# Kernel optimization log

Measured on AMD Instinct MI355X. Metric: run time of the kernel, lower is better.

## Reference

```python
import jax, jax.numpy as jnp
import numpy as np

SIGMA = 1.0
EPS = 1e-5
NEG = 0.1
CPG = 16  # channels_per_group


def bn(x, g, b):
    # batch norm over the point dimension (training-mode batch stats)
    m = x.mean(0, keepdims=True)
    v = x.var(0, keepdims=True)
    return (x - m) / jnp.sqrt(v + EPS) * g + b


def lrelu(x):
    return jnp.where(x >= 0, x, NEG * x)


def kpinv_conv(q_pts, s_pts, x, idx, kp, w_g1, b_g1, w_g2, b_g2):
    # KPInv: neighbor gather + kernel-point influence weighting + dynamically
    # generated (involution-style) per-point, per-kernel, per-group weights.
    M, H = idx.shape
    K = kp.shape[0]
    C = x.shape[1]
    G = C // CPG
    # shadow padding: far-away point, zero feature
    s_pts_p = jnp.concatenate([s_pts, jnp.full((1, s_pts.shape[1]), 1e6, s_pts.dtype)], 0)
    x_p = jnp.concatenate([x, jnp.zeros((1, C), x.dtype)], 0)
    npts = s_pts_p[idx] - q_pts[:, None, :]              # (M,H,D) relative neighbor positions
    nfeat = x_p[idx]                                      # (M,H,C) gathered neighbor features
    # squared distances to kernel points without materializing (M,H,K,D)
    d2 = ((npts ** 2).sum(-1)[:, :, None]
          + (kp ** 2).sum(-1)[None, None, :]
          - 2.0 * jnp.einsum('mhd,kd->mhk', npts, kp))    # (M,H,K)
    # linear influence, sum aggregation
    infl = jnp.clip(1.0 - jnp.sqrt(jnp.maximum(d2, 0.0)) / SIGMA, 0.0, None)
    fk = jnp.einsum('mhk,mhc->mkc', infl, nfeat)          # (M,K,C) per-kernel aggregated feats
    # generate conv weights from local max-pooled center feature
    center = jnp.max(nfeat, axis=1)                       # (M,C)
    w = lrelu(center @ w_g1 + b_g1) @ w_g2 + b_g2         # (M,K*G)
    w = w.reshape(M, K, G)
    fk = fk.reshape(M, K, G, CPG)
    return jnp.einsum('mkg,mkgc->mgc', w, fk).reshape(M, C)


def setup_inputs() -> dict:
    key = jax.random.key(0)
    ks = jax.random.split(key, 10)
    M, H, Cin, Cmid, K, D = 50000, 32, 128, 32, 15, 3
    R = 2.5
    pts = jax.random.uniform(ks[0], (M, D), dtype=jnp.float32) * 10.0
    return dict(
        q_pts=pts,
        s_pts=pts,
        s_feats=jax.random.normal(ks[1], (M, Cin), dtype=jnp.float32),
        neighbor_indices=jax.random.randint(ks[2], (M, H), 0, M),
        kernel_points=jax.random.normal(ks[3], (K, D), dtype=jnp.float32) * (0.3 * R),
        w_u1=jax.random.normal(ks[4], (Cin, Cmid), dtype=jnp.float32) / np.float32(np.sqrt(Cin)),
        g_u1=jnp.ones((Cmid,), jnp.float32), b_u1=jnp.zeros((Cmid,), jnp.float32),
        w_g1=jax.random.normal(ks[5], (Cmid, Cmid // 4), dtype=jnp.float32) / np.float32(np.sqrt(Cmid)),
        b_g1=jnp.zeros((Cmid // 4,), jnp.float32),
        w_g2=jax.random.normal(ks[6], (Cmid // 4, K * (Cmid // CPG)), dtype=jnp.float32) / np.float32(np.sqrt(Cmid // 4)),
        b_g2=jnp.zeros((K * (Cmid // CPG),), jnp.float32),
        g_c=jnp.ones((Cmid,), jnp.float32), b_c=jnp.zeros((Cmid,), jnp.float32),
        w_u2=jax.random.normal(ks[7], (Cmid, Cin), dtype=jnp.float32) / np.float32(np.sqrt(Cmid)),
        g_u2=jnp.ones((Cin,), jnp.float32), b_u2=jnp.zeros((Cin,), jnp.float32),
    )


def reference(q_pts, s_pts, s_feats, neighbor_indices, kernel_points,
              w_u1, g_u1, b_u1, w_g1, b_g1, w_g2, b_g2,
              g_c, b_c, w_u2, g_u2, b_u2):
    # unary1: linear -> BN -> LeakyReLU (in_channels != mid_channels)
    x = lrelu(bn(s_feats @ w_u1, g_u1, b_u1))
    # KPInv conv block: conv -> BN -> LeakyReLU
    x = kpinv_conv(q_pts, s_pts, x, neighbor_indices, kernel_points, w_g1, b_g1, w_g2, b_g2)
    x = lrelu(bn(x, g_c, b_c))
    # unary2: linear -> BN (no activation)
    x = bn(x @ w_u2, g_u2, b_u2)
    # not strided, in==out: shortcut is identity on s_feats
    return lrelu(x + s_feats)
```

## Files before the change

kernel.cpp:

```cpp
#include <hip/hip_runtime.h>

#define CMID 32
#define CIN 128
#define HNB 32
#define KP 15
#define NEG 0.1f
#define EPS 1e-5f

__global__ __launch_bounds__(256) void k1_gemm1(
    const float* __restrict__ A,
    const float* __restrict__ B,
    float* __restrict__ y1,
    float* __restrict__ st,
    int M)
{
    __shared__ __align__(16) float AsT[32 * 128];
    __shared__ __align__(16) float Bs[128 * 32];
    __shared__ __align__(16) float red[256];
    int t = threadIdx.x;
    for (int i = t; i < 128 * 32; i += 256) Bs[i] = B[i];

    int m0 = blockIdx.x * 128;
    int tx = t & 7, ty = t >> 3;
    int srow = t & 127, shh = t >> 7;
    float acc[4][4] = {{0.f}};

    for (int ch = 0; ch < 4; ++ch) {
        __syncthreads();
        int gr = m0 + srow;
        const float4* ap = (const float4*)(A + (size_t)gr * CIN + ch * 32 + shh * 16);
        float4 f0, f1, f2, f3;
        if (gr < M) { f0 = ap[0]; f1 = ap[1]; f2 = ap[2]; f3 = ap[3]; }
        else { f0 = f1 = f2 = f3 = make_float4(0.f, 0.f, 0.f, 0.f); }
        {
            int cb = shh * 16;
            AsT[(cb + 0) * 128 + srow] = f0.x;  AsT[(cb + 1) * 128 + srow] = f0.y;
            AsT[(cb + 2) * 128 + srow] = f0.z;  AsT[(cb + 3) * 128 + srow] = f0.w;
            AsT[(cb + 4) * 128 + srow] = f1.x;  AsT[(cb + 5) * 128 + srow] = f1.y;
            AsT[(cb + 6) * 128 + srow] = f1.z;  AsT[(cb + 7) * 128 + srow] = f1.w;
            AsT[(cb + 8) * 128 + srow] = f2.x;  AsT[(cb + 9) * 128 + srow] = f2.y;
            AsT[(cb + 10) * 128 + srow] = f2.z; AsT[(cb + 11) * 128 + srow] = f2.w;
            AsT[(cb + 12) * 128 + srow] = f3.x; AsT[(cb + 13) * 128 + srow] = f3.y;
            AsT[(cb + 14) * 128 + srow] = f3.z; AsT[(cb + 15) * 128 + srow] = f3.w;
        }
        __syncthreads();
        const float* bsp = Bs + (ch * 32) * 32 + tx * 4;
#pragma unroll
        for (int jl = 0; jl < 32; ++jl) {
            float4 av = *(const float4*)(AsT + jl * 128 + ty * 4);
            float4 bv = *(const float4*)(bsp + jl * 32);
            acc[0][0] += av.x * bv.x; acc[0][1] += av.x * bv.y; acc[0][2] += av.x * bv.z; acc[0][3] += av.x * bv.w;
            acc[1][0] += av.y * bv.x; acc[1][1] += av.y * bv.y; acc[1][2] += av.y * bv.z; acc[1][3] += av.y * bv.w;
            acc[2][0] += av.z * bv.x; acc[2][1] += av.z * bv.y; acc[2][2] += av.z * bv.z; acc[2][3] += av.z * bv.w;
            acc[3][0] += av.w * bv.x; acc[3][1] += av.w * bv.y; acc[3][2] += av.w * bv.z; acc[3][3] += av.w * bv.w;
        }
    }
#pragma unroll
    for (int i = 0; i < 4; ++i) {
        int r = m0 + ty * 4 + i;
        if (r < M)
            *(float4*)(y1 + (size_t)r * CMID + tx * 4) =
                make_float4(acc[i][0], acc[i][1], acc[i][2], acc[i][3]);
    }
    float s4[4], q4[4];
#pragma unroll
    for (int e = 0; e < 4; ++e) {
        s4[e] = acc[0][e] + acc[1][e] + acc[2][e] + acc[3][e];
        q4[e] = acc[0][e] * acc[0][e] + acc[1][e] * acc[1][e]
              + acc[2][e] * acc[2][e] + acc[3][e] * acc[3][e];
    }
#pragma unroll
    for (int off = 8; off <= 32; off <<= 1) {
#pragma unroll
        for (int e = 0; e < 4; ++e) {
            s4[e] += __shfl_xor(s4[e], off);
            q4[e] += __shfl_xor(q4[e], off);
        }
    }
    int lw = t >> 6, ll = t & 63;
    if (ll < 8) {
#pragma unroll
        for (int e = 0; e < 4; ++e) {
            red[(lw * 8 + ll) * 8 + e] = s4[e];
            red[(lw * 8 + ll) * 8 + 4 + e] = q4[e];
        }
    }
    __syncthreads();
    if (t < 64) {
        int tx2 = t >> 3, k = t & 7;
        float v = red[(0 * 8 + tx2) * 8 + k] + red[(1 * 8 + tx2) * 8 + k]
                + red[(2 * 8 + tx2) * 8 + k] + red[(3 * 8 + tx2) * 8 + k];
        int col = tx2 * 4 + (k & 3);
        atomicAdd(&st[(k < 4 ? 0 : 32) + col], v);
    }
}

__global__ __launch_bounds__(256, 4) void k3_kpinv(
    const float* __restrict__ y1, const float* __restrict__ st,
    const float* __restrict__ q_pts, const float* __restrict__ s_pts,
    const int* __restrict__ idx, const float* __restrict__ kp,
    const float* __restrict__ g_u1, const float* __restrict__ b_u1,
    const float* __restrict__ w_g1, const float* __restrict__ b_g1,
    const float* __restrict__ w_g2, const float* __restrict__ b_g2,
    float* __restrict__ x2, int M)
{
    __shared__ __align__(16) float a1s[32], b1s[32];
    __shared__ __align__(16) float wg1[32 * 8];
    __shared__ __align__(16) float bg1[8];
    __shared__ __align__(16) float wg2[8 * 30];
    __shared__ __align__(16) float bg2[32];
    __shared__ __align__(16) float kps[KP * 3 + 1];
    __shared__ __align__(16) float vbuf[4][2][32 * 32];
    __shared__ __align__(16) float aux[4][2][144];

    int t = threadIdx.x;
    if (t < 32) {
        float mean = st[t] * (1.0f / M);
        float var  = st[32 + t] * (1.0f / M) - mean * mean;
        float inv  = rsqrtf(var + EPS);
        float a = g_u1[t] * inv;
        a1s[t] = a;
        b1s[t] = b_u1[t] - mean * a;
    }
    wg1[t & 255] = w_g1[t & 255];
    if (t < 8)   bg1[t] = b_g1[t];
    if (t < 240) wg2[t] = w_g2[t];
    if (t < 30)  bg2[t] = b_g2[t];
    else if (t < 32) bg2[t] = 0.f;
    if (t < KP * 3) kps[t] = kp[t];
    __syncthreads();

    int wave = t >> 6, lane = t & 63;
    int p = lane >> 5;
    int q = lane & 31;
    int m = blockIdx.x * 8 + wave * 2 + p;
    bool valid = (m < M);
    int mm = valid ? m : 0;
    float* vb = &vbuf[wave][p][0];
    float* ax = &aux[wave][p][0];

    int h = q;
    int n = idx[(size_t)mm * HNB + h];
    float qx = q_pts[mm * 3 + 0], qy = q_pts[mm * 3 + 1], qz = q_pts[mm * 3 + 2];
    float dx = s_pts[n * 3 + 0] - qx;
    float dy = s_pts[n * 3 + 1] - qy;
    float dz = s_pts[n * 3 + 2] - qz;

    float infl[KP];
#pragma unroll
    for (int k = 0; k < KP; ++k) {
        float ex = dx - kps[k * 3 + 0];
        float ey = dy - kps[k * 3 + 1];
        float ez = dz - kps[k * 3 + 2];
        float d = sqrtf(ex * ex + ey * ey + ez * ez);
        infl[k] = fmaxf(1.0f - d, 0.f);
    }

    {
        const float4* row = (const float4*)(y1 + (size_t)n * CMID);
        int hq4 = h >> 2, h3 = h & 3;
#pragma unroll
        for (int jj = 0; jj < 8; ++jj) {
            float4 f = row[jj];
            float vv[4] = {f.x, f.y, f.z, f.w};
#pragma unroll
            for (int e = 0; e < 4; ++e) {
                int c = jj * 4 + e;
                float x = vv[e] * a1s[c] + b1s[c];
                x = fmaxf(x, NEG * x);
                vb[(c << 5) + ((hq4 ^ (c & 7)) << 2) + h3] = x;
            }
        }
    }
    __builtin_amdgcn_wave_barrier();

    {
        int c = q;
        int c7 = c & 7;
        const float* vrow = vb + (c << 5);
        float cm = -1e30f;
#pragma unroll
        for (int j = 0; j < 8; ++j) {
            const float4 f = *(const float4*)(vrow + ((j ^ c7) << 2));
            cm = fmaxf(fmaxf(fmaxf(cm, f.x), fmaxf(f.y, f.z)), f.w);
        }
        ax[c] = cm;
        __builtin_amdgcn_wave_barrier();

        int jm = c & 7;
        float acc = bg1[jm];
#pragma unroll
        for (int cc = 0; cc < 8; ++cc) {
            const float4 ce = *(const float4*)(ax + (cc << 2));
            acc += ce.x * wg1[(cc * 4 + 0) * 8 + jm];
            acc += ce.y * wg1[(cc * 4 + 1) * 8 + jm];
            acc += ce.z * wg1[(cc * 4 + 2) * 8 + jm];
            acc += ce.w * wg1[(cc * 4 + 3) * 8 + jm];
        }
        float h1v = fmaxf(acc, NEG * acc);
        if (c < 8) ax[32 + c] = h1v;
        __builtin_amdgcn_wave_barrier();

        float wv = 0.f;
        if (c < 30) {
            const float4 ha = *(const float4*)(ax + 32);
            const float4 hb = *(const float4*)(ax + 36);
            wv = bg2[c]
               + ha.x * wg2[0 * 30 + c] + ha.y * wg2[1 * 30 + c]
               + ha.z * wg2[2 * 30 + c] + ha.w * wg2[3 * 30 + c]
               + hb.x * wg2[4 * 30 + c] + hb.y * wg2[5 * 30 + c]
               + hb.z * wg2[6 * 30 + c] + hb.w * wg2[7 * 30 + c];
        }
        ax[40 + c] = wv;
    }
    __builtin_amdgcn_wave_barrier();

    {
        float wf[32];
#pragma unroll
        for (int j = 0; j < 8; ++j) {
            const float4 wc = *(const float4*)(ax + 40 + (j << 2));
            wf[j * 4 + 0] = wc.x; wf[j * 4 + 1] = wc.y;
            wf[j * 4 + 2] = wc.z; wf[j * 4 + 3] = wc.w;
        }
        float s0 = 0.f, s1 = 0.f;
#pragma unroll
        for (int k = 0; k < KP; ++k) {
            s0 += infl[k] * wf[2 * k + 0];
            s1 += infl[k] * wf[2 * k + 1];
        }
        ax[72 + q]  = s0;
        ax[104 + q] = s1;
    }
    __builtin_amdgcn_wave_barrier();

    {
        int c = q;
        int c7 = c & 7;
        const float* sbuf = ax + 72 + ((c >> 4) << 5);
        const float* vrow = vb + (c << 5);
        float o = 0.f;
#pragma unroll
        for (int j = 0; j < 8; ++j) {
            const float4 vv = *(const float4*)(vrow + ((j ^ c7) << 2));
            const float4 ss = *(const float4*)(sbuf + (j << 2));
            o += vv.x * ss.x + vv.y * ss.y + vv.z * ss.z + vv.w * ss.w;
        }
        if (valid) x2[(size_t)m * CMID + c] = o;
    }
}

__global__ __launch_bounds__(256) void k4_stats32(
    const float* __restrict__ x2, float* __restrict__ st, int M)
{
    int t = threadIdx.x;
    int c = t & 31;
    float sum = 0.f, sq = 0.f;
    for (int r = blockIdx.x * 8 + (t >> 5); r < M; r += gridDim.x * 8) {
        float v = x2[(size_t)r * CMID + c];
        sum += v; sq += v * v;
    }
    __shared__ float red[256];
    red[t] = sum; __syncthreads();
    if (t < 32) { float s = 0.f; for (int i = 0; i < 8; ++i) s += red[t + 32 * i]; atomicAdd(&st[64 + t], s); }
    __syncthreads();
    red[t] = sq; __syncthreads();
    if (t < 32) { float s = 0.f; for (int i = 0; i < 8; ++i) s += red[t + 32 * i]; atomicAdd(&st[96 + t], s); }
}

__global__ __launch_bounds__(256) void k6_zstats(
    const float* __restrict__ x2, const float* __restrict__ w_u2,
    const float* __restrict__ g_c, const float* __restrict__ b_c,
    float* __restrict__ st, int M)
{
    __shared__ __align__(16) float ST[32 * 128];
    __shared__ __align__(16) float Ws[32 * 32];
    __shared__ __align__(16) float acs[32], bcs[32];
    __shared__ __align__(16) float red[256];
    int t = threadIdx.x;
    int cb = blockIdx.y;
    int m0 = blockIdx.x * 128;
    if (t < 32) {
        float mean = st[64 + t] * (1.0f / M);
        float var  = st[96 + t] * (1.0f / M) - mean * mean;
        float inv  = rsqrtf(var + EPS);
        float a = g_c[t] * inv;
        acs[t] = a; bcs[t] = b_c[t] - mean * a;
    }
    for (int i = t; i < 32 * 32; i += 256)
        Ws[i] = w_u2[(i >> 5) * CIN + cb * 32 + (i & 31)];
    __syncthreads();

    int srow = t & 127, shh = t >> 7;
    int gr = m0 + srow;
    const float4* xp = (const float4*)(x2 + (size_t)gr * CMID + shh * 16);
    float4 f0, f1, f2, f3;
    if (gr < M) { f0 = xp[0]; f1 = xp[1]; f2 = xp[2]; f3 = xp[3]; }
    else { f0 = f1 = f2 = f3 = make_float4(0.f, 0.f, 0.f, 0.f); }
    {
        float vv[16] = {f0.x, f0.y, f0.z, f0.w, f1.x, f1.y, f1.z, f1.w,
                        f2.x, f2.y, f2.z, f2.w, f3.x, f3.y, f3.z, f3.w};
        int cbse = shh * 16;
#pragma unroll
        for (int e = 0; e < 16; ++e) {
            int c = cbse + e;
            float x = vv[e] * acs[c] + bcs[c];
            x = fmaxf(x, NEG * x);
            ST[c * 128 + srow] = (gr < M) ? x : 0.f;
        }
    }
    __syncthreads();

    int tx = t & 7, ty = t >> 3;
    float acc[4][4] = {{0.f}};
#pragma unroll
    for (int j = 0; j < 32; ++j) {
        float4 av = *(const float4*)(ST + j * 128 + ty * 4);
        float4 bv = *(const float4*)(Ws + j * 32 + tx * 4);
        acc[0][0] += av.x * bv.x; acc[0][1] += av.x * bv.y; acc[0][2] += av.x * bv.z; acc[0][3] += av.x * bv.w;
        acc[1][0] += av.y * bv.x; acc[1][1] += av.y * bv.y; acc[1][2] += av.y * bv.z; acc[1][3] += av.y * bv.w;
        acc[2][0] += av.z * bv.x; acc[2][1] += av.z * bv.y; acc[2][2] += av.z * bv.z; acc[2][3] += av.z * bv.w;
        acc[3][0] += av.w * bv.x; acc[3][1] += av.w * bv.y; acc[3][2] += av.w * bv.z; acc[3][3] += av.w * bv.w;
    }
    float s4[4], q4[4];
#pragma unroll
    for (int e = 0; e < 4; ++e) {
        s4[e] = acc[0][e] + acc[1][e] + acc[2][e] + acc[3][e];
        q4[e] = acc[0][e] * acc[0][e] + acc[1][e] * acc[1][e]
              + acc[2][e] * acc[2][e] + acc[3][e] * acc[3][e];
    }
#pragma unroll
    for (int off = 8; off <= 32; off <<= 1) {
#pragma unroll
        for (int e = 0; e < 4; ++e) {
            s4[e] += __shfl_xor(s4[e], off);
            q4[e] += __shfl_xor(q4[e], off);
        }
    }
    int lw = t >> 6, ll = t & 63;
    if (ll < 8) {
#pragma unroll
        for (int e = 0; e < 4; ++e) {
            red[(lw * 8 + ll) * 8 + e] = s4[e];
            red[(lw * 8 + ll) * 8 + 4 + e] = q4[e];
        }
    }
    __syncthreads();
    if (t < 64) {
        int tx2 = t >> 3, k = t & 7;
        float v = red[(0 * 8 + tx2) * 8 + k] + red[(1 * 8 + tx2) * 8 + k]
                + red[(2 * 8 + tx2) * 8 + k] + red[(3 * 8 + tx2) * 8 + k];
        int col = cb * 32 + tx2 * 4 + (k & 3);
        atomicAdd(&st[(k < 4 ? 128 : 256) + col], v);
    }
}

__global__ __launch_bounds__(256) void k8_final(
    const float* __restrict__ x2, const float* __restrict__ w_u2,
    const float* __restrict__ g_c, const float* __restrict__ b_c,
    const float* __restrict__ g_u2, const float* __restrict__ b_u2,
    const float* __restrict__ s_feats, const float* __restrict__ st,
    float* __restrict__ out, int M)
{
    __shared__ __align__(16) float ST[32 * 128];
    __shared__ __align__(16) float Ws[32 * 32];
    __shared__ __align__(16) float acs[32], bcs[32];
    __shared__ __align__(16) float a2s[32], b2s[32];
    int t = threadIdx.x;
    int cb = blockIdx.y;
    int m0 = blockIdx.x * 128;
    if (t < 32) {
        float mean = st[64 + t] * (1.0f / M);
        float var  = st[96 + t] * (1.0f / M) - mean * mean;
        float inv  = rsqrtf(var + EPS);
        float a = g_c[t] * inv;
        acs[t] = a; bcs[t] = b_c[t] - mean * a;
        int c = cb * 32 + t;
        float mean2 = st[128 + c] * (1.0f / M);
        float var2  = st[256 + c] * (1.0f / M) - mean2 * mean2;
        float inv2  = rsqrtf(var2 + EPS);
        float a2 = g_u2[c] * inv2;
        a2s[t] = a2; b2s[t] = b_u2[c] - mean2 * a2;
    }
    for (int i = t; i < 32 * 32; i += 256)
        Ws[i] = w_u2[(i >> 5) * CIN + cb * 32 + (i & 31)];
    __syncthreads();

    int srow = t & 127, shh = t >> 7;
    int gr = m0 + srow;
    const float4* xp = (const float4*)(x2 + (size_t)gr * CMID + shh * 16);
    float4 f0, f1, f2, f3;
    if (gr < M) { f0 = xp[0]; f1 = xp[1]; f2 = xp[2]; f3 = xp[3]; }
    else { f0 = f1 = f2 = f3 = make_float4(0.f, 0.f, 0.f, 0.f); }
    {
        float vv[16] = {f0.x, f0.y, f0.z, f0.w, f1.x, f1.y, f1.z, f1.w,
                        f2.x, f2.y, f2.z, f2.w, f3.x, f3.y, f3.z, f3.w};
        int cbse = shh * 16;
#pragma unroll
        for (int e = 0; e < 16; ++e) {
            int c = cbse + e;
            float x = vv[e] * acs[c] + bcs[c];
            x = fmaxf(x, NEG * x);
            ST[c * 128 + srow] = (gr < M) ? x : 0.f;
        }
    }
    __syncthreads();

    int tx = t & 7, ty = t >> 3;
    float acc[4][4] = {{0.f}};
#pragma unroll
    for (int j = 0; j < 32; ++j) {
        float4 av = *(const float4*)(ST + j * 128 + ty * 4);
        float4 bv = *(const float4*)(Ws + j * 32 + tx * 4);
        acc[0][0] += av.x * bv.x; acc[0][1] += av.x * bv.y; acc[0][2] += av.x * bv.z; acc[0][3] += av.x * bv.w;
        acc[1][0] += av.y * bv.x; acc[1][1] += av.y * bv.y; acc[1][2] += av.y * bv.z; acc[1][3] += av.y * bv.w;
        acc[2][0] += av.z * bv.x; acc[2][1] += av.z * bv.y; acc[2][2] += av.z * bv.z; acc[2][3] += av.z * bv.w;
        acc[3][0] += av.w * bv.x; acc[3][1] += av.w * bv.y; acc[3][2] += av.w * bv.z; acc[3][3] += av.w * bv.w;
    }
    int lc = tx * 4;
    float a0 = a2s[lc + 0], a1 = a2s[lc + 1], a2v = a2s[lc + 2], a3 = a2s[lc + 3];
    float bb0 = b2s[lc + 0], bb1 = b2s[lc + 1], bb2 = b2s[lc + 2], bb3 = b2s[lc + 3];
#pragma unroll
    for (int i = 0; i < 4; ++i) {
        int r = m0 + ty * 4 + i;
        if (r < M) {
            size_t gi = (size_t)r * CIN + cb * 32 + lc;
            float4 sf = *(const float4*)(s_feats + gi);
            float v0 = acc[i][0] * a0 + bb0 + sf.x;
            float v1 = acc[i][1] * a1 + bb1 + sf.y;
            float v2 = acc[i][2] * a2v + bb2 + sf.z;
            float v3 = acc[i][3] * a3 + bb3 + sf.w;
            v0 = fmaxf(v0, NEG * v0); v1 = fmaxf(v1, NEG * v1);
            v2 = fmaxf(v2, NEG * v2); v3 = fmaxf(v3, NEG * v3);
            *(float4*)(out + gi) = make_float4(v0, v1, v2, v3);
        }
    }
}

extern "C" void kernel_launch(void* const* d_in, const int* in_sizes, int n_in,
                              void* d_out, int out_size, void* d_ws, size_t ws_size,
                              hipStream_t stream) {
    const float* q_pts   = (const float*)d_in[0];
    const float* s_pts   = (const float*)d_in[1];
    const float* s_feats = (const float*)d_in[2];
    const int*   idx     = (const int*)d_in[3];
    const float* kp      = (const float*)d_in[4];
    const float* w_u1    = (const float*)d_in[5];
    const float* g_u1    = (const float*)d_in[6];
    const float* b_u1    = (const float*)d_in[7];
    const float* w_g1    = (const float*)d_in[8];
    const float* b_g1    = (const float*)d_in[9];
    const float* w_g2    = (const float*)d_in[10];
    const float* b_g2    = (const float*)d_in[11];
    const float* g_c     = (const float*)d_in[12];
    const float* b_c     = (const float*)d_in[13];
    const float* w_u2    = (const float*)d_in[14];
    const float* g_u2    = (const float*)d_in[15];
    const float* b_u2    = (const float*)d_in[16];

    int M = in_sizes[3] / HNB;

    float* ws = (float*)d_ws;
    float* y1 = ws;
    float* x2 = ws + (size_t)M * CMID;
    float* st = ws + (size_t)M * 2 * CMID;

    hipMemsetAsync(st, 0, 384 * sizeof(float), stream);

    int nbr = (M + 127) / 128;
    k1_gemm1<<<nbr, 256, 0, stream>>>(s_feats, w_u1, y1, st, M);
    k3_kpinv<<<(M + 7) / 8, 256, 0, stream>>>(y1, st, q_pts, s_pts, idx, kp,
                                              g_u1, b_u1, w_g1, b_g1, w_g2, b_g2,
                                              x2, M);
    k4_stats32<<<128, 256, 0, stream>>>(x2, st, M);
    k6_zstats<<<dim3(nbr, 4), 256, 0, stream>>>(x2, w_u2, g_c, b_c, st, M);
    k8_final<<<dim3(nbr, 4), 256, 0, stream>>>(x2, w_u2, g_c, b_c, g_u2, b_u2,
                                               s_feats, st, (float*)d_out, M);
}
```

Before: 253.0 us.

## Fuse all stages into one persistent kernel with software grid barriers

Replaces the five separate kernel launches with a single persistent kernel of fixed grid size that loops over row tiles in each phase. The phases are separated by atomic-counter grid barriers, and the shared-memory buffers for each phase are overlaid in a union. This is meant to remove launch gaps and kernel-boundary drains. In exchange it relies on all blocks being co-resident, since otherwise the barriers deadlock, and it loses parallelism in phases that previously used far more blocks.

```diff
diff --git a/kernel.cpp b/kernel.cpp
--- a/kernel.cpp
+++ b/kernel.cpp
@@ -6,433 +6,441 @@
 #define KP 15
 #define NEG 0.1f
 #define EPS 1e-5f
-
-__global__ __launch_bounds__(256) void k1_gemm1(
-    const float* __restrict__ A,
-    const float* __restrict__ B,
-    float* __restrict__ y1,
-    float* __restrict__ st,
-    int M)
+#define GRID 512
+#define GQ (GRID / 4)
+
+__device__ __forceinline__ void grid_barrier(unsigned int* bar, unsigned int target, int t)
 {
-    __shared__ __align__(16) float AsT[32 * 128];
-    __shared__ __align__(16) float Bs[128 * 32];
-    __shared__ __align__(16) float red[256];
-    int t = threadIdx.x;
-    for (int i = t; i < 128 * 32; i += 256) Bs[i] = B[i];
-
-    int m0 = blockIdx.x * 128;
-    int tx = t & 7, ty = t >> 3;
-    int srow = t & 127, shh = t >> 7;
-    float acc[4][4] = {{0.f}};
-
-    for (int ch = 0; ch < 4; ++ch) {
-        __syncthreads();
-        int gr = m0 + srow;
-        const float4* ap = (const float4*)(A + (size_t)gr * CIN + ch * 32 + shh * 16);
-        float4 f0, f1, f2, f3;
-        if (gr < M) { f0 = ap[0]; f1 = ap[1]; f2 = ap[2]; f3 = ap[3]; }
-        else { f0 = f1 = f2 = f3 = make_float4(0.f, 0.f, 0.f, 0.f); }
-        {
-            int cb = shh * 16;
-            AsT[(cb + 0) * 128 + srow] = f0.x;  AsT[(cb + 1) * 128 + srow] = f0.y;
-            AsT[(cb + 2) * 128 + srow] = f0.z;  AsT[(cb + 3) * 128 + srow] = f0.w;
-            AsT[(cb + 4) * 128 + srow] = f1.x;  AsT[(cb + 5) * 128 + srow] = f1.y;
-            AsT[(cb + 6) * 128 + srow] = f1.z;  AsT[(cb + 7) * 128 + srow] = f1.w;
-            AsT[(cb + 8) * 128 + srow] = f2.x;  AsT[(cb + 9) * 128 + srow] = f2.y;
-            AsT[(cb + 10) * 128 + srow] = f2.z; AsT[(cb + 11) * 128 + srow] = f2.w;
-            AsT[(cb + 12) * 128 + srow] = f3.x; AsT[(cb + 13) * 128 + srow] = f3.y;
-            AsT[(cb + 14) * 128 + srow] = f3.z; AsT[(cb + 15) * 128 + srow] = f3.w;
-        }
-        __syncthreads();
-        const float* bsp = Bs + (ch * 32) * 32 + tx * 4;
-#pragma unroll
-        for (int jl = 0; jl < 32; ++jl) {
-            float4 av = *(const float4*)(AsT + jl * 128 + ty * 4);
-            float4 bv = *(const float4*)(bsp + jl * 32);
-            acc[0][0] += av.x * bv.x; acc[0][1] += av.x * bv.y; acc[0][2] += av.x * bv.z; acc[0][3] += av.x * bv.w;
-            acc[1][0] += av.y * bv.x; acc[1][1] += av.y * bv.y; acc[1][2] += av.y * bv.z; acc[1][3] += av.y * bv.w;
-            acc[2][0] += av.z * bv.x; acc[2][1] += av.z * bv.y; acc[2][2] += av.z * bv.z; acc[2][3] += av.z * bv.w;
-            acc[3][0] += av.w * bv.x; acc[3][1] += av.w * bv.y; acc[3][2] += av.w * bv.z; acc[3][3] += av.w * bv.w;
-        }
-    }
-#pragma unroll
-    for (int i = 0; i < 4; ++i) {
-        int r = m0 + ty * 4 + i;
-        if (r < M)
-            *(float4*)(y1 + (size_t)r * CMID + tx * 4) =
-                make_float4(acc[i][0], acc[i][1], acc[i][2], acc[i][3]);
-    }
-    float s4[4], q4[4];
-#pragma unroll
-    for (int e = 0; e < 4; ++e) {
-        s4[e] = acc[0][e] + acc[1][e] + acc[2][e] + acc[3][e];
-        q4[e] = acc[0][e] * acc[0][e] + acc[1][e] * acc[1][e]
-              + acc[2][e] * acc[2][e] + acc[3][e] * acc[3][e];
-    }
-#pragma unroll
-    for (int off = 8; off <= 32; off <<= 1) {
-#pragma unroll
-        for (int e = 0; e < 4; ++e) {
-            s4[e] += __shfl_xor(s4[e], off);
-            q4[e] += __shfl_xor(q4[e], off);
-        }
-    }
-    int lw = t >> 6, ll = t & 63;
-    if (ll < 8) {
-#pragma unroll
-        for (int e = 0; e < 4; ++e) {
-            red[(lw * 8 + ll) * 8 + e] = s4[e];
-            red[(lw * 8 + ll) * 8 + 4 + e] = q4[e];
-        }
+    __threadfence();
+    __syncthreads();
+    if (t == 0) {
+        __hip_atomic_fetch_add(bar, 1u, __ATOMIC_RELEASE, __HIP_MEMORY_SCOPE_AGENT);
+        while (__hip_atomic_load(bar, __ATOMIC_ACQUIRE, __HIP_MEMORY_SCOPE_AGENT) < target)
+            __builtin_amdgcn_s_sleep(8);
     }
     __syncthreads();
-    if (t < 64) {
-        int tx2 = t >> 3, k = t & 7;
-        float v = red[(0 * 8 + tx2) * 8 + k] + red[(1 * 8 + tx2) * 8 + k]
-                + red[(2 * 8 + tx2) * 8 + k] + red[(3 * 8 + tx2) * 8 + k];
-        int col = tx2 * 4 + (k & 3);
-        atomicAdd(&st[(k < 4 ? 0 : 32) + col], v);
-    }
 }
 
-__global__ __launch_bounds__(256, 4) void k3_kpinv(
-    const float* __restrict__ y1, const float* __restrict__ st,
+struct SA {
+    float AsT[32 * 128];
+    float Bs[128 * 32];
+    float red[256];
+};
+struct SB {
+    float a1s[32], b1s[32];
+    float wg1[32 * 8];
+    float bg1[8];
+    float wg2[8 * 30];
+    float bg2[32];
+    float kps[48];
+    float vbuf[4][2][1024];
+    float aux[4][2][144];
+};
+struct SD {
+    float ST[32 * 128];
+    float Ws[32 * 32];
+    float acs[32], bcs[32];
+    float a2s[32], b2s[32];
+    float red[256];
+};
+union SU { SA a; SB b; SD d; };
+
+__global__ __launch_bounds__(256, 3) void fused(
     const float* __restrict__ q_pts, const float* __restrict__ s_pts,
-    const int* __restrict__ idx, const float* __restrict__ kp,
-    const float* __restrict__ g_u1, const float* __restrict__ b_u1,
+    const float* __restrict__ s_feats, const int* __restrict__ idx,
+    const float* __restrict__ kp,
+    const float* __restrict__ w_u1, const float* __restrict__ g_u1,
+    const float* __restrict__ b_u1,
     const float* __restrict__ w_g1, const float* __restrict__ b_g1,
     const float* __restrict__ w_g2, const float* __restrict__ b_g2,
-    float* __restrict__ x2, int M)
-{
-    __shared__ __align__(16) float a1s[32], b1s[32];
-    __shared__ __align__(16) float wg1[32 * 8];
-    __shared__ __align__(16) float bg1[8];
-    __shared__ __align__(16) float wg2[8 * 30];
-    __shared__ __align__(16) float bg2[32];
-    __shared__ __align__(16) float kps[KP * 3 + 1];
-    __shared__ __align__(16) float vbuf[4][2][32 * 32];
-    __shared__ __align__(16) float aux[4][2][144];
-
-    int t = threadIdx.x;
-    if (t < 32) {
-        float mean = st[t] * (1.0f / M);
-        float var  = st[32 + t] * (1.0f / M) - mean * mean;
-        float inv  = rsqrtf(var + EPS);
-        float a = g_u1[t] * inv;
-        a1s[t] = a;
-        b1s[t] = b_u1[t] - mean * a;
-    }
-    wg1[t & 255] = w_g1[t & 255];
-    if (t < 8)   bg1[t] = b_g1[t];
-    if (t < 240) wg2[t] = w_g2[t];
-    if (t < 30)  bg2[t] = b_g2[t];
-    else if (t < 32) bg2[t] = 0.f;
-    if (t < KP * 3) kps[t] = kp[t];
-    __syncthreads();
-
-    int wave = t >> 6, lane = t & 63;
-    int p = lane >> 5;
-    int q = lane & 31;
-    int m = blockIdx.x * 8 + wave * 2 + p;
-    bool valid = (m < M);
-    int mm = valid ? m : 0;
-    float* vb = &vbuf[wave][p][0];
-    float* ax = &aux[wave][p][0];
-
-    int h = q;
-    int n = idx[(size_t)mm * HNB + h];
-    float qx = q_pts[mm * 3 + 0], qy = q_pts[mm * 3 + 1], qz = q_pts[mm * 3 + 2];
-    float dx = s_pts[n * 3 + 0] - qx;
-    float dy = s_pts[n * 3 + 1] - qy;
-    float dz = s_pts[n * 3 + 2] - qz;
-
-    float infl[KP];
-#pragma unroll
-    for (int k = 0; k < KP; ++k) {
-        float ex = dx - kps[k * 3 + 0];
-        float ey = dy - kps[k * 3 + 1];
-        float ez = dz - kps[k * 3 + 2];
-        float d = sqrtf(ex * ex + ey * ey + ez * ez);
-        infl[k] = fmaxf(1.0f - d, 0.f);
-    }
-
-    {
-        const float4* row = (const float4*)(y1 + (size_t)n * CMID);
-        int hq4 = h >> 2, h3 = h & 3;
-#pragma unroll
-        for (int jj = 0; jj < 8; ++jj) {
-            float4 f = row[jj];
-            float vv[4] = {f.x, f.y, f.z, f.w};
-#pragma unroll
-            for (int e = 0; e < 4; ++e) {
-                int c = jj * 4 + e;
-                float x = vv[e] * a1s[c] + b1s[c];
-                x = fmaxf(x, NEG * x);
-                vb[(c << 5) + ((hq4 ^ (c & 7)) << 2) + h3] = x;
-            }
-        }
-    }
-    __builtin_amdgcn_wave_barrier();
-
-    {
-        int c = q;
-        int c7 = c & 7;
-        const float* vrow = vb + (c << 5);
-        float cm = -1e30f;
-#pragma unroll
-        for (int j = 0; j < 8; ++j) {
-            const float4 f = *(const float4*)(vrow + ((j ^ c7) << 2));
-            cm = fmaxf(fmaxf(fmaxf(cm, f.x), fmaxf(f.y, f.z)), f.w);
-        }
-        ax[c] = cm;
-        __builtin_amdgcn_wave_barrier();
-
-        int jm = c & 7;
-        float acc = bg1[jm];
-#pragma unroll
-        for (int cc = 0; cc < 8; ++cc) {
-            const float4 ce = *(const float4*)(ax + (cc << 2));
-            acc += ce.x * wg1[(cc * 4 + 0) * 8 + jm];
-            acc += ce.y * wg1[(cc * 4 + 1) * 8 + jm];
-            acc += ce.z * wg1[(cc * 4 + 2) * 8 + jm];
-            acc += ce.w * wg1[(cc * 4 + 3) * 8 + jm];
-        }
-        float h1v = fmaxf(acc, NEG * acc);
-        if (c < 8) ax[32 + c] = h1v;
-        __builtin_amdgcn_wave_barrier();
-
-        float wv = 0.f;
-        if (c < 30) {
-            const float4 ha = *(const float4*)(ax + 32);
-            const float4 hb = *(const float4*)(ax + 36);
-            wv = bg2[c]
-               + ha.x * wg2[0 * 30 + c] + ha.y * wg2[1 * 30 + c]
-               + ha.z * wg2[2 * 30 + c] + ha.w * wg2[3 * 30 + c]
-               + hb.x * wg2[4 * 30 + c] + hb.y * wg2[5 * 30 + c]
-               + hb.z * wg2[6 * 30 + c] + hb.w * wg2[7 * 30 + c];
-        }
-        ax[40 + c] = wv;
-    }
-    __builtin_amdgcn_wave_barrier();
-
-    {
-        float wf[32];
-#pragma unroll
-        for (int j = 0; j < 8; ++j) {
-            const float4 wc = *(const float4*)(ax + 40 + (j << 2));
-            wf[j * 4 + 0] = wc.x; wf[j * 4 + 1] = wc.y;
-            wf[j * 4 + 2] = wc.z; wf[j * 4 + 3] = wc.w;
-        }
-        float s0 = 0.f, s1 = 0.f;
-#pragma unroll
-        for (int k = 0; k < KP; ++k) {
-            s0 += infl[k] * wf[2 * k + 0];
-            s1 += infl[k] * wf[2 * k + 1];
-        }
-        ax[72 + q]  = s0;
-        ax[104 + q] = s1;
-    }
-    __builtin_amdgcn_wave_barrier();
-
-    {
-        int c = q;
-        int c7 = c & 7;
-        const float* sbuf = ax + 72 + ((c >> 4) << 5);
-        const float* vrow = vb + (c << 5);
-        float o = 0.f;
-#pragma unroll
-        for (int j = 0; j < 8; ++j) {
-            const float4 vv = *(const float4*)(vrow + ((j ^ c7) << 2));
-            const float4 ss = *(const float4*)(sbuf + (j << 2));
-            o += vv.x * ss.x + vv.y * ss.y + vv.z * ss.z + vv.w * ss.w;
-        }
-        if (valid) x2[(size_t)m * CMID + c] = o;
-    }
-}
-
-__global__ __launch_bounds__(256) void k4_stats32(
-    const float* __restrict__ x2, float* __restrict__ st, int M)
-{
-    int t = threadIdx.x;
-    int c = t & 31;
-    float sum = 0.f, sq = 0.f;
-    for (int r = blockIdx.x * 8 + (t >> 5); r < M; r += gridDim.x * 8) {
-        float v = x2[(size_t)r * CMID + c];
-        sum += v; sq += v * v;
-    }
-    __shared__ float red[256];
-    red[t] = sum; __syncthreads();
-    if (t < 32) { float s = 0.f; for (int i = 0; i < 8; ++i) s += red[t + 32 * i]; atomicAdd(&st[64 + t], s); }
-    __syncthreads();
-    red[t] = sq; __syncthreads();
-    if (t < 32) { float s = 0.f; for (int i = 0; i < 8; ++i) s += red[t + 32 * i]; atomicAdd(&st[96 + t], s); }
-}
-
-__global__ __launch_bounds__(256) void k6_zstats(
-    const float* __restrict__ x2, const float* __restrict__ w_u2,
     const float* __restrict__ g_c, const float* __restrict__ b_c,
-    float* __restrict__ st, int M)
-{
-    __shared__ __align__(16) float ST[32 * 128];
-    __shared__ __align__(16) float Ws[32 * 32];
-    __shared__ __align__(16) float acs[32], bcs[32];
-    __shared__ __align__(16) float red[256];
-    int t = threadIdx.x;
-    int cb = blockIdx.y;
-    int m0 = blockIdx.x * 128;
-    if (t < 32) {
-        float mean = st[64 + t] * (1.0f / M);
-        float var  = st[96 + t] * (1.0f / M) - mean * mean;
-        float inv  = rsqrtf(var + EPS);
-        float a = g_c[t] * inv;
-        acs[t] = a; bcs[t] = b_c[t] - mean * a;
-    }
-    for (int i = t; i < 32 * 32; i += 256)
-        Ws[i] = w_u2[(i >> 5) * CIN + cb * 32 + (i & 31)];
-    __syncthreads();
-
-    int srow = t & 127, shh = t >> 7;
-    int gr = m0 + srow;
-    const float4* xp = (const float4*)(x2 + (size_t)gr * CMID + shh * 16);
-    float4 f0, f1, f2, f3;
-    if (gr < M) { f0 = xp[0]; f1 = xp[1]; f2 = xp[2]; f3 = xp[3]; }
-    else { f0 = f1 = f2 = f3 = make_float4(0.f, 0.f, 0.f, 0.f); }
-    {
-        float vv[16] = {f0.x, f0.y, f0.z, f0.w, f1.x, f1.y, f1.z, f1.w,
-                        f2.x, f2.y, f2.z, f2.w, f3.x, f3.y, f3.z, f3.w};
-        int cbse = shh * 16;
-#pragma unroll
-        for (int e = 0; e < 16; ++e) {
-            int c = cbse + e;
-            float x = vv[e] * acs[c] + bcs[c];
-            x = fmaxf(x, NEG * x);
-            ST[c * 128 + srow] = (gr < M) ? x : 0.f;
-        }
-    }
-    __syncthreads();
-
-    int tx = t & 7, ty = t >> 3;
-    float acc[4][4] = {{0.f}};
-#pragma unroll
-    for (int j = 0; j < 32; ++j) {
-        float4 av = *(const float4*)(ST + j * 128 + ty * 4);
-        float4 bv = *(const float4*)(Ws + j * 32 + tx * 4);
-        acc[0][0] += av.x * bv.x; acc[0][1] += av.x * bv.y; acc[0][2] += av.x * bv.z; acc[0][3] += av.x * bv.w;
-        acc[1][0] += av.y * bv.x; acc[1][1] += av.y * bv.y; acc[1][2] += av.y * bv.z; acc[1][3] += av.y * bv.w;
-        acc[2][0] += av.z * bv.x; acc[2][1] += av.z * bv.y; acc[2][2] += av.z * bv.z; acc[2][3] += av.z * bv.w;
-        acc[3][0] += av.w * bv.x; acc[3][1] += av.w * bv.y; acc[3][2] += av.w * bv.z; acc[3][3] += av.w * bv.w;
-    }
-    float s4[4], q4[4];
-#pragma unroll
-    for (int e = 0; e < 4; ++e) {
-        s4[e] = acc[0][e] + acc[1][e] + acc[2][e] + acc[3][e];
-        q4[e] = acc[0][e] * acc[0][e] + acc[1][e] * acc[1][e]
-              + acc[2][e] * acc[2][e] + acc[3][e] * acc[3][e];
-    }
-#pragma unroll
-    for (int off = 8; off <= 32; off <<= 1) {
-#pragma unroll
-        for (int e = 0; e < 4; ++e) {
-            s4[e] += __shfl_xor(s4[e], off);
-            q4[e] += __shfl_xor(q4[e], off);
-        }
-    }
-    int lw = t >> 6, ll = t & 63;
-    if (ll < 8) {
-#pragma unroll
-        for (int e = 0; e < 4; ++e) {
-            red[(lw * 8 + ll) * 8 + e] = s4[e];
-            red[(lw * 8 + ll) * 8 + 4 + e] = q4[e];
-        }
-    }
-    __syncthreads();
-    if (t < 64) {
-        int tx2 = t >> 3, k = t & 7;
-        float v = red[(0 * 8 + tx2) * 8 + k] + red[(1 * 8 + tx2) * 8 + k]
-                + red[(2 * 8 + tx2) * 8 + k] + red[(3 * 8 + tx2) * 8 + k];
-        int col = cb * 32 + tx2 * 4 + (k & 3);
-        atomicAdd(&st[(k < 4 ? 128 : 256) + col], v);
-    }
-}
-
-__global__ __launch_bounds__(256) void k8_final(
-    const float* __restrict__ x2, const float* __restrict__ w_u2,
-    const float* __restrict__ g_c, const float* __restrict__ b_c,
-    const float* __restrict__ g_u2, const float* __restrict__ b_u2,
-    const float* __restrict__ s_feats, const float* __restrict__ st,
+    const float* __restrict__ w_u2, const float* __restrict__ g_u2,
+    const float* __restrict__ b_u2,
+    float* __restrict__ y1, float* __restrict__ x2, float* __restrict__ st,
+    unsigned int* __restrict__ bar,
     float* __restrict__ out, int M)
 {
-    __shared__ __align__(16) float ST[32 * 128];
-    __shared__ __align__(16) float Ws[32 * 32];
-    __shared__ __align__(16) float acs[32], bcs[32];
-    __shared__ __align__(16) float a2s[32], b2s[32];
+    __shared__ __align__(16) SU sm;
     int t = threadIdx.x;
-    int cb = blockIdx.y;
-    int m0 = blockIdx.x * 128;
-    if (t < 32) {
-        float mean = st[64 + t] * (1.0f / M);
-        float var  = st[96 + t] * (1.0f / M) - mean * mean;
-        float inv  = rsqrtf(var + EPS);
-        float a = g_c[t] * inv;
-        acs[t] = a; bcs[t] = b_c[t] - mean * a;
-        int c = cb * 32 + t;
-        float mean2 = st[128 + c] * (1.0f / M);
-        float var2  = st[256 + c] * (1.0f / M) - mean2 * mean2;
-        float inv2  = rsqrtf(var2 + EPS);
-        float a2 = g_u2[c] * inv2;
-        a2s[t] = a2; b2s[t] = b_u2[c] - mean2 * a2;
+    int nb1 = (M + 127) / 128;
+
+    {
+        for (int i = t; i < 128 * 32; i += 256) sm.a.Bs[i] = w_u1[i];
+        int tx = t & 7, ty = t >> 3;
+        int srow = t & 127, shh = t >> 7;
+        for (int bb = blockIdx.x; bb < nb1; bb += GRID) {
+            int m0 = bb * 128;
+            float acc[4][4] = {{0.f}};
+            for (int ch = 0; ch < 4; ++ch) {
+                __syncthreads();
+                int gr = m0 + srow;
+                const float4* ap = (const float4*)(s_feats + (size_t)gr * CIN + ch * 32 + shh * 16);
+                float4 f0, f1, f2, f3;
+                if (gr < M) { f0 = ap[0]; f1 = ap[1]; f2 = ap[2]; f3 = ap[3]; }
+                else { f0 = f1 = f2 = f3 = make_float4(0.f, 0.f, 0.f, 0.f); }
+                int cb = shh * 16;
+                sm.a.AsT[(cb + 0) * 128 + srow] = f0.x;  sm.a.AsT[(cb + 1) * 128 + srow] = f0.y;
+                sm.a.AsT[(cb + 2) * 128 + srow] = f0.z;  sm.a.AsT[(cb + 3) * 128 + srow] = f0.w;
+                sm.a.AsT[(cb + 4) * 128 + srow] = f1.x;  sm.a.AsT[(cb + 5) * 128 + srow] = f1.y;
+                sm.a.AsT[(cb + 6) * 128 + srow] = f1.z;  sm.a.AsT[(cb + 7) * 128 + srow] = f1.w;
+                sm.a.AsT[(cb + 8) * 128 + srow] = f2.x;  sm.a.AsT[(cb + 9) * 128 + srow] = f2.y;
+                sm.a.AsT[(cb + 10) * 128 + srow] = f2.z; sm.a.AsT[(cb + 11) * 128 + srow] = f2.w;
+                sm.a.AsT[(cb + 12) * 128 + srow] = f3.x; sm.a.AsT[(cb + 13) * 128 + srow] = f3.y;
+                sm.a.AsT[(cb + 14) * 128 + srow] = f3.z; sm.a.AsT[(cb + 15) * 128 + srow] = f3.w;
+                __syncthreads();
+                const float* bsp = sm.a.Bs + (ch * 32) * 32 + tx * 4;
+#pragma unroll
+                for (int jl = 0; jl < 32; ++jl) {
+                    float4 av = *(const float4*)(sm.a.AsT + jl * 128 + ty * 4);
+                    float4 bv = *(const float4*)(bsp + jl * 32);
+                    acc[0][0] += av.x * bv.x; acc[0][1] += av.x * bv.y; acc[0][2] += av.x * bv.z; acc[0][3] += av.x * bv.w;
+                    acc[1][0] += av.y * bv.x; acc[1][1] += av.y * bv.y; acc[1][2] += av.y * bv.z; acc[1][3] += av.y * bv.w;
+                    acc[2][0] += av.z * bv.x; acc[2][1] += av.z * bv.y; acc[2][2] += av.z * bv.z; acc[2][3] += av.z * bv.w;
+                    acc[3][0] += av.w * bv.x; acc[3][1] += av.w * bv.y; acc[3][2] += av.w * bv.z; acc[3][3] += av.w * bv.w;
+                }
+            }
+#pragma unroll
+            for (int i = 0; i < 4; ++i) {
+                int r = m0 + ty * 4 + i;
+                if (r < M)
+                    *(float4*)(y1 + (size_t)r * CMID + tx * 4) =
+                        make_float4(acc[i][0], acc[i][1], acc[i][2], acc[i][3]);
+            }
+            float s4[4], q4[4];
+#pragma unroll
+            for (int e = 0; e < 4; ++e) {
+                s4[e] = acc[0][e] + acc[1][e] + acc[2][e] + acc[3][e];
+                q4[e] = acc[0][e] * acc[0][e] + acc[1][e] * acc[1][e]
+                      + acc[2][e] * acc[2][e] + acc[3][e] * acc[3][e];
+            }
+#pragma unroll
+            for (int off = 8; off <= 32; off <<= 1) {
+#pragma unroll
+                for (int e = 0; e < 4; ++e) {
+                    s4[e] += __shfl_xor(s4[e], off);
+                    q4[e] += __shfl_xor(q4[e], off);
+                }
+            }
+            int lw = t >> 6, ll = t & 63;
+            if (ll < 8) {
+#pragma unroll
+                for (int e = 0; e < 4; ++e) {
+                    sm.a.red[(lw * 8 + ll) * 8 + e] = s4[e];
+                    sm.a.red[(lw * 8 + ll) * 8 + 4 + e] = q4[e];
+                }
+            }
+            __syncthreads();
+            if (t < 64) {
+                int tx2 = t >> 3, k = t & 7;
+                float v = sm.a.red[(0 * 8 + tx2) * 8 + k] + sm.a.red[(1 * 8 + tx2) * 8 + k]
+                        + sm.a.red[(2 * 8 + tx2) * 8 + k] + sm.a.red[(3 * 8 + tx2) * 8 + k];
+                int col = tx2 * 4 + (k & 3);
+                atomicAdd(&st[(k < 4 ? 0 : 32) + col], v);
+            }
+        }
     }
-    for (int i = t; i < 32 * 32; i += 256)
-        Ws[i] = w_u2[(i >> 5) * CIN + cb * 32 + (i & 31)];
-    __syncthreads();
-
-    int srow = t & 127, shh = t >> 7;
-    int gr = m0 + srow;
-    const float4* xp = (const float4*)(x2 + (size_t)gr * CMID + shh * 16);
-    float4 f0, f1, f2, f3;
-    if (gr < M) { f0 = xp[0]; f1 = xp[1]; f2 = xp[2]; f3 = xp[3]; }
-    else { f0 = f1 = f2 = f3 = make_float4(0.f, 0.f, 0.f, 0.f); }
+    grid_barrier(bar, GRID, t);
+
     {
-        float vv[16] = {f0.x, f0.y, f0.z, f0.w, f1.x, f1.y, f1.z, f1.w,
-                        f2.x, f2.y, f2.z, f2.w, f3.x, f3.y, f3.z, f3.w};
-        int cbse = shh * 16;
-#pragma unroll
-        for (int e = 0; e < 16; ++e) {
-            int c = cbse + e;
-            float x = vv[e] * acs[c] + bcs[c];
-            x = fmaxf(x, NEG * x);
-            ST[c * 128 + srow] = (gr < M) ? x : 0.f;
-        }
+        if (t < 32) {
+            float mean = st[t] * (1.0f / M);
+            float var  = st[32 + t] * (1.0f / M) - mean * mean;
+            float inv  = rsqrtf(var + EPS);
+            float a = g_u1[t] * inv;
+            sm.b.a1s[t] = a;
+            sm.b.b1s[t] = b_u1[t] - mean * a;
+        }
+        sm.b.wg1[t] = w_g1[t];
+        if (t < 8)   sm.b.bg1[t] = b_g1[t];
+        if (t < 240) sm.b.wg2[t] = w_g2[t];
+        if (t < 30)  sm.b.bg2[t] = b_g2[t];
+        else if (t < 32) sm.b.bg2[t] = 0.f;
+        if (t < KP * 3) sm.b.kps[t] = kp[t];
+        __syncthreads();
+
+        int wave = t >> 6, lane = t & 63;
+        int p = lane >> 5;
+        int q = lane & 31;
+        float* vb = &sm.b.vbuf[wave][p][0];
+        float* ax = &sm.b.aux[wave][p][0];
+        float ssum = 0.f, ssq = 0.f;
+        int ng = (M + 7) / 8;
+
+        for (int g = blockIdx.x; g < ng; g += GRID) {
+            int m = g * 8 + wave * 2 + p;
+            bool valid = (m < M);
+            int mm = valid ? m : 0;
+
+            int h = q;
+            int n = idx[(size_t)mm * HNB + h];
+            float qx = q_pts[mm * 3 + 0], qy = q_pts[mm * 3 + 1], qz = q_pts[mm * 3 + 2];
+            float dx = s_pts[n * 3 + 0] - qx;
+            float dy = s_pts[n * 3 + 1] - qy;
+            float dz = s_pts[n * 3 + 2] - qz;
+            float infl[KP];
+#pragma unroll
+            for (int k = 0; k < KP; ++k) {
+                float ex = dx - sm.b.kps[k * 3 + 0];
+                float ey = dy - sm.b.kps[k * 3 + 1];
+                float ez = dz - sm.b.kps[k * 3 + 2];
+                float d = sqrtf(ex * ex + ey * ey + ez * ez);
+                infl[k] = fmaxf(1.0f - d, 0.f);
+            }
+            {
+                const float4* row = (const float4*)(y1 + (size_t)n * CMID);
+                int hq4 = h >> 2, h3 = h & 3;
+#pragma unroll
+                for (int jj = 0; jj < 8; ++jj) {
+                    float4 f = row[jj];
+                    float vv[4] = {f.x, f.y, f.z, f.w};
+#pragma unroll
+                    for (int e = 0; e < 4; ++e) {
+                        int c = jj * 4 + e;
+                        float x = vv[e] * sm.b.a1s[c] + sm.b.b1s[c];
+                        x = fmaxf(x, NEG * x);
+                        vb[(c << 5) + ((hq4 ^ (c & 7)) << 2) + h3] = x;
+                    }
+                }
+            }
+            __builtin_amdgcn_wave_barrier();
+
+            {
+                int c = q;
+                int c7 = c & 7;
+                const float* vrow = vb + (c << 5);
+                float cm = -1e30f;
+#pragma unroll
+                for (int j = 0; j < 8; ++j) {
+                    const float4 f = *(const float4*)(vrow + ((j ^ c7) << 2));
+                    cm = fmaxf(fmaxf(fmaxf(cm, f.x), fmaxf(f.y, f.z)), f.w);
+                }
+                ax[c] = cm;
+                __builtin_amdgcn_wave_barrier();
+
+                int jm = c & 7;
+                float acc = sm.b.bg1[jm];
+#pragma unroll
+                for (int cc = 0; cc < 8; ++cc) {
+                    const float4 ce = *(const float4*)(ax + (cc << 2));
+                    acc += ce.x * sm.b.wg1[(cc * 4 + 0) * 8 + jm];
+                    acc += ce.y * sm.b.wg1[(cc * 4 + 1) * 8 + jm];
+                    acc += ce.z * sm.b.wg1[(cc * 4 + 2) * 8 + jm];
+                    acc += ce.w * sm.b.wg1[(cc * 4 + 3) * 8 + jm];
+                }
+                float h1v = fmaxf(acc, NEG * acc);
+                if (c < 8) ax[32 + c] = h1v;
+                __builtin_amdgcn_wave_barrier();
+
+                float wv = 0.f;
+                if (c < 30) {
+                    const float4 ha = *(const float4*)(ax + 32);
+                    const float4 hb = *(const float4*)(ax + 36);
+                    wv = sm.b.bg2[c]
+                       + ha.x * sm.b.wg2[0 * 30 + c] + ha.y * sm.b.wg2[1 * 30 + c]
+                       + ha.z * sm.b.wg2[2 * 30 + c] + ha.w * sm.b.wg2[3 * 30 + c]
+                       + hb.x * sm.b.wg2[4 * 30 + c] + hb.y * sm.b.wg2[5 * 30 + c]
+                       + hb.z * sm.b.wg2[6 * 30 + c] + hb.w * sm.b.wg2[7 * 30 + c];
+                }
+                ax[40 + c] = wv;
+            }
+            __builtin_amdgcn_wave_barrier();
+
+            {
+                float wf[32];
+#pragma unroll
+                for (int j = 0; j < 8; ++j) {
+                    const float4 wc = *(const float4*)(ax + 40 + (j << 2));
+                    wf[j * 4 + 0] = wc.x; wf[j * 4 + 1] = wc.y;
+                    wf[j * 4 + 2] = wc.z; wf[j * 4 + 3] = wc.w;
+                }
+                float s0 = 0.f, s1 = 0.f;
+#pragma unroll
+                for (int k = 0; k < KP; ++k) {
+                    s0 += infl[k] * wf[2 * k + 0];
+                    s1 += infl[k] * wf[2 * k + 1];
+                }
+                ax[72 + q]  = s0;
+                ax[104 + q] = s1;
+            }
+            __builtin_amdgcn_wave_barrier();
+
+            {
+                int c = q;
+                int c7 = c & 7;
+                const float* sbuf = ax + 72 + ((c >> 4) << 5);
+                const float* vrow = vb + (c << 5);
+                float o = 0.f;
+#pragma unroll
+                for (int j = 0; j < 8; ++j) {
+                    const float4 vv = *(const float4*)(vrow + ((j ^ c7) << 2));
+                    const float4 ss = *(const float4*)(sbuf + (j << 2));
+                    o += vv.x * ss.x + vv.y * ss.y + vv.z * ss.z + vv.w * ss.w;
+                }
+                if (valid) {
+                    x2[(size_t)m * CMID + c] = o;
+                    ssum += o; ssq += o * o;
+                }
+            }
+            __builtin_amdgcn_wave_barrier();
+        }
+        __syncthreads();
+        float* red2 = (float*)&sm;
+        red2[t] = ssum; __syncthreads();
+        if (t < 32) { float s = 0.f; for (int i = 0; i < 8; ++i) s += red2[t + 32 * i]; atomicAdd(&st[64 + t], s); }
+        __syncthreads();
+        red2[t] = ssq; __syncthreads();
+        if (t < 32) { float s = 0.f; for (int i = 0; i < 8; ++i) s += red2[t + 32 * i]; atomicAdd(&st[96 + t], s); }
     }
-    __syncthreads();
-
-    int tx = t & 7, ty = t >> 3;
-    float acc[4][4] = {{0.f}};
-#pragma unroll
-    for (int j = 0; j < 32; ++j) {
-        float4 av = *(const float4*)(ST + j * 128 + ty * 4);
-        float4 bv = *(const float4*)(Ws + j * 32 + tx * 4);
-        acc[0][0] += av.x * bv.x; acc[0][1] += av.x * bv.y; acc[0][2] += av.x * bv.z; acc[0][3] += av.x * bv.w;
-        acc[1][0] += av.y * bv.x; acc[1][1] += av.y * bv.y; acc[1][2] += av.y * bv.z; acc[1][3] += av.y * bv.w;
-        acc[2][0] += av.z * bv.x; acc[2][1] += av.z * bv.y; acc[2][2] += av.z * bv.z; acc[2][3] += av.z * bv.w;
-        acc[3][0] += av.w * bv.x; acc[3][1] += av.w * bv.y; acc[3][2] += av.w * bv.z; acc[3][3] += av.w * bv.w;
+    grid_barrier(bar, 2 * GRID, t);
+
+    int cb3 = blockIdx.x & 3;
+    {
+        if (t < 32) {
+            float mean = st[64 + t] * (1.0f / M);
+            float var  = st[96 + t] * (1.0f / M) - mean * mean;
+            float inv  = rsqrtf(var + EPS);
+            float a = g_c[t] * inv;
+            sm.d.acs[t] = a; sm.d.bcs[t] = b_c[t] - mean * a;
+        }
+        for (int i = t; i < 32 * 32; i += 256)
+            sm.d.Ws[i] = w_u2[(i >> 5) * CIN + cb3 * 32 + (i & 31)];
+
+        int srow = t & 127, shh = t >> 7;
+        int tx = t & 7, ty = t >> 3;
+        for (int bbr = blockIdx.x >> 2; bbr < nb1; bbr += GQ) {
+            int m0 = bbr * 128;
+            __syncthreads();
+            int gr = m0 + srow;
+            const float4* xp = (const float4*)(x2 + (size_t)gr * CMID + shh * 16);
+            float4 f0, f1, f2, f3;
+            if (gr < M) { f0 = xp[0]; f1 = xp[1]; f2 = xp[2]; f3 = xp[3]; }
+            else { f0 = f1 = f2 = f3 = make_float4(0.f, 0.f, 0.f, 0.f); }
+            {
+                float vv[16] = {f0.x, f0.y, f0.z, f0.w, f1.x, f1.y, f1.z, f1.w,
+                                f2.x, f2.y, f2.z, f2.w, f3.x, f3.y, f3.z, f3.w};
+                int cbse = shh * 16;
+#pragma unroll
+                for (int e = 0; e < 16; ++e) {
+                    int c = cbse + e;
+                    float x = vv[e] * sm.d.acs[c] + sm.d.bcs[c];
+                    x = fmaxf(x, NEG * x);
+                    sm.d.ST[c * 128 + srow] = (gr < M) ? x : 0.f;
+                }
+            }
+            __syncthreads();
+            float acc[4][4] = {{0.f}};
+#pragma unroll
+            for (int j = 0; j < 32; ++j) {
+                float4 av = *(const float4*)(sm.d.ST + j * 128 + ty * 4);
+                float4 bv = *(const float4*)(sm.d.Ws + j * 32 + tx * 4);
+                acc[0][0] += av.x * bv.x; acc[0][1] += av.x * bv.y; acc[0][2] += av.x * bv.z; acc[0][3] += av.x * bv.w;
+                acc[1][0] += av.y * bv.x; acc[1][1] += av.y * bv.y; acc[1][2] += av.y * bv.z; acc[1][3] += av.y * bv.w;
+                acc[2][0] += av.z * bv.x; acc[2][1] += av.z * bv.y; acc[2][2] += av.z * bv.z; acc[2][3] += av.z * bv.w;
+                acc[3][0] += av.w * bv.x; acc[3][1] += av.w * bv.y; acc[3][2] += av.w * bv.z; acc[3][3] += av.w * bv.w;
+            }
+            float s4[4], q4[4];
+#pragma unroll
+            for (int e = 0; e < 4; ++e) {
+                s4[e] = acc[0][e] + acc[1][e] + acc[2][e] + acc[3][e];
+                q4[e] = acc[0][e] * acc[0][e] + acc[1][e] * acc[1][e]
+                      + acc[2][e] * acc[2][e] + acc[3][e] * acc[3][e];
+            }
+#pragma unroll
+            for (int off = 8; off <= 32; off <<= 1) {
+#pragma unroll
+                for (int e = 0; e < 4; ++e) {
+                    s4[e] += __shfl_xor(s4[e], off);
+                    q4[e] += __shfl_xor(q4[e], off);
+                }
+            }
+            int lw = t >> 6, ll = t & 63;
+            if (ll < 8) {
+#pragma unroll
+                for (int e = 0; e < 4; ++e) {
+                    sm.d.red[(lw * 8 + ll) * 8 + e] = s4[e];
+                    sm.d.red[(lw * 8 + ll) * 8 + 4 + e] = q4[e];
+                }
+            }
+            __syncthreads();
+            if (t < 64) {
+                int tx2 = t >> 3, k = t & 7;
+                float v = sm.d.red[(0 * 8 + tx2) * 8 + k] + sm.d.red[(1 * 8 + tx2) * 8 + k]
+                        + sm.d.red[(2 * 8 + tx2) * 8 + k] + sm.d.red[(3 * 8 + tx2) * 8 + k];
+                int col = cb3 * 32 + tx2 * 4 + (k & 3);
+                atomicAdd(&st[(k < 4 ? 128 : 256) + col], v);
+            }
+        }
     }
-    int lc = tx * 4;
-    float a0 = a2s[lc + 0], a1 = a2s[lc + 1], a2v = a2s[lc + 2], a3 = a2s[lc + 3];
-    float bb0 = b2s[lc + 0], bb1 = b2s[lc + 1], bb2 = b2s[lc + 2], bb3 = b2s[lc + 3];
-#pragma unroll
-    for (int i = 0; i < 4; ++i) {
-        int r = m0 + ty * 4 + i;
-        if (r < M) {
-            size_t gi = (size_t)r * CIN + cb * 32 + lc;
-            float4 sf = *(const float4*)(s_feats + gi);
-            float v0 = acc[i][0] * a0 + bb0 + sf.x;
-            float v1 = acc[i][1] * a1 + bb1 + sf.y;
-            float v2 = acc[i][2] * a2v + bb2 + sf.z;
-            float v3 = acc[i][3] * a3 + bb3 + sf.w;
-            v0 = fmaxf(v0, NEG * v0); v1 = fmaxf(v1, NEG * v1);
-            v2 = fmaxf(v2, NEG * v2); v3 = fmaxf(v3, NEG * v3);
-            *(float4*)(out + gi) = make_float4(v0, v1, v2, v3);
+    grid_barrier(bar, 3 * GRID, t);
+
+    {
+        if (t < 32) {
+            float mean = st[64 + t] * (1.0f / M);
+            float var  = st[96 + t] * (1.0f / M) - mean * mean;
+            float inv  = rsqrtf(var + EPS);
+            float a = g_c[t] * inv;
+            sm.d.acs[t] = a; sm.d.bcs[t] = b_c[t] - mean * a;
+            int c = cb3 * 32 + t;
+            float mean2 = st[128 + c] * (1.0f / M);
+            float var2  = st[256 + c] * (1.0f / M) - mean2 * mean2;
+            float inv2  = rsqrtf(var2 + EPS);
+            float a2 = g_u2[c] * inv2;
+            sm.d.a2s[t] = a2; sm.d.b2s[t] = b_u2[c] - mean2 * a2;
+        }
+        for (int i = t; i < 32 * 32; i += 256)
+            sm.d.Ws[i] = w_u2[(i >> 5) * CIN + cb3 * 32 + (i & 31)];
+
+        int srow = t & 127, shh = t >> 7;
+        int tx = t & 7, ty = t >> 3;
+        for (int bbr = blockIdx.x >> 2; bbr < nb1; bbr += GQ) {
+            int m0 = bbr * 128;
+            __syncthreads();
+            int gr = m0 + srow;
+            const float4* xp = (const float4*)(x2 + (size_t)gr * CMID + shh * 16);
+            float4 f0, f1, f2, f3;
+            if (gr < M) { f0 = xp[0]; f1 = xp[1]; f2 = xp[2]; f3 = xp[3]; }
+            else { f0 = f1 = f2 = f3 = make_float4(0.f, 0.f, 0.f, 0.f); }
+            {
+                float vv[16] = {f0.x, f0.y, f0.z, f0.w, f1.x, f1.y, f1.z, f1.w,
+                                f2.x, f2.y, f2.z, f2.w, f3.x, f3.y, f3.z, f3.w};
+                int cbse = shh * 16;
+#pragma unroll
+                for (int e = 0; e < 16; ++e) {
+                    int c = cbse + e;
+                    float x = vv[e] * sm.d.acs[c] + sm.d.bcs[c];
+                    x = fmaxf(x, NEG * x);
+                    sm.d.ST[c * 128 + srow] = (gr < M) ? x : 0.f;
+                }
+            }
+            __syncthreads();
+            float acc[4][4] = {{0.f}};
+#pragma unroll
+            for (int j = 0; j < 32; ++j) {
+                float4 av = *(const float4*)(sm.d.ST + j * 128 + ty * 4);
+                float4 bv = *(const float4*)(sm.d.Ws + j * 32 + tx * 4);
+                acc[0][0] += av.x * bv.x; acc[0][1] += av.x * bv.y; acc[0][2] += av.x * bv.z; acc[0][3] += av.x * bv.w;
+                acc[1][0] += av.y * bv.x; acc[1][1] += av.y * bv.y; acc[1][2] += av.y * bv.z; acc[1][3] += av.y * bv.w;
+                acc[2][0] += av.z * bv.x; acc[2][1] += av.z * bv.y; acc[2][2] += av.z * bv.z; acc[2][3] += av.z * bv.w;
+                acc[3][0] += av.w * bv.x; acc[3][1] += av.w * bv.y; acc[3][2] += av.w * bv.z; acc[3][3] += av.w * bv.w;
+            }
+            int lc = tx * 4;
+            float a0 = sm.d.a2s[lc + 0], a1 = sm.d.a2s[lc + 1], a2v = sm.d.a2s[lc + 2], a3 = sm.d.a2s[lc + 3];
+            float bb0 = sm.d.b2s[lc + 0], bb1 = sm.d.b2s[lc + 1], bb2 = sm.d.b2s[lc + 2], bb3 = sm.d.b2s[lc + 3];
+#pragma unroll
+            for (int i = 0; i < 4; ++i) {
+                int r = m0 + ty * 4 + i;
+                if (r < M) {
+                    size_t gi = (size_t)r * CIN + cb3 * 32 + lc;
+                    float4 sf = *(const float4*)(s_feats + gi);
+                    float v0 = acc[i][0] * a0 + bb0 + sf.x;
+                    float v1 = acc[i][1] * a1 + bb1 + sf.y;
+                    float v2 = acc[i][2] * a2v + bb2 + sf.z;
+                    float v3 = acc[i][3] * a3 + bb3 + sf.w;
+                    v0 = fmaxf(v0, NEG * v0); v1 = fmaxf(v1, NEG * v1);
+                    v2 = fmaxf(v2, NEG * v2); v3 = fmaxf(v3, NEG * v3);
+                    *(float4*)(out + gi) = make_float4(v0, v1, v2, v3);
+                }
+            }
         }
     }
 }
@@ -464,16 +472,13 @@
     float* y1 = ws;
     float* x2 = ws + (size_t)M * CMID;
     float* st = ws + (size_t)M * 2 * CMID;
-
-    hipMemsetAsync(st, 0, 384 * sizeof(float), stream);
-
-    int nbr = (M + 127) / 128;
-    k1_gemm1<<<nbr, 256, 0, stream>>>(s_feats, w_u1, y1, st, M);
-    k3_kpinv<<<(M + 7) / 8, 256, 0, stream>>>(y1, st, q_pts, s_pts, idx, kp,
-                                              g_u1, b_u1, w_g1, b_g1, w_g2, b_g2,
-                                              x2, M);
-    k4_stats32<<<128, 256, 0, stream>>>(x2, st, M);
-    k6_zstats<<<dim3(nbr, 4), 256, 0, stream>>>(x2, w_u2, g_c, b_c, st, M);
-    k8_final<<<dim3(nbr, 4), 256, 0, stream>>>(x2, w_u2, g_c, b_c, g_u2, b_u2,
-                                               s_feats, st, (float*)d_out, M);
+    unsigned int* bar = (unsigned int*)(st + 384);
+
+    hipMemsetAsync(st, 0, 512 * sizeof(float), stream);
+
+    fused<<<GRID, 256, 0, stream>>>(
+        q_pts, s_pts, s_feats, idx, kp,
+        w_u1, g_u1, b_u1, w_g1, b_g1, w_g2, b_g2,
+        g_c, b_c, w_u2, g_u2, b_u2,
+        y1, x2, st, bar, (float*)d_out, M);
 }
```

New measurement: 565.9 us. 124% more time.
